# Performance work log

Hardware: AMD Instinct MI355X
Metric: run time of the kernel (lower is better)

The kernel has to match this reference:

```python
import jax, jax.numpy as jnp
import numpy as np

N_KNOTS = 16384
BATCH = 256
N_SAMP = 32768


def setup_inputs() -> dict:
    key = jax.random.key(0)
    k1, k2, k3 = jax.random.split(key, 3)
    # strictly increasing knot abscissae (matches module assumption of sorted x_points)
    incs = jax.random.uniform(k1, (N_KNOTS,), minval=0.01, maxval=1.0, dtype=jnp.float32)
    x_points = jnp.cumsum(incs)
    y_points = jax.random.normal(k2, (N_KNOTS,), dtype=jnp.float32)
    # samples must have a valid right bracket: x in [x_points[0], x_points[N-2])
    lo = x_points[0]
    hi = x_points[N_KNOTS - 2]
    u = jax.random.uniform(k3, (BATCH, N_SAMP), dtype=jnp.float32)
    x_samp = lo + u * (hi - lo) * 0.999
    return {"x_samp": x_samp, "x_points": x_points, "y_points": y_points}


def reference(x_samp, x_points, y_points):
    # Original: masked argmin over (x_samp - x_points) with negatives set to inf,
    # i.e. index of the largest knot <= x_samp. Equivalent to searchsorted(right)-1.
    idxi = jnp.searchsorted(x_points, x_samp, side='right') - 1  # [B, S]
    idxf = idxi + 1
    xi = x_points[idxi]  # [B, S] gather
    xf = x_points[idxf]
    yi = y_points[idxi]
    yf = y_points[idxf]
    ds = (x_samp - xi) / (xf - xi)
    return yi + ds * (yf - yi)
```

## Files before the change

kernel.cpp:

```cpp
#include <hip/hip_runtime.h>


#define NB 16256
#define NKMAX 16384
#define PADR 4
#define NREC (NKMAX + PADR)

typedef float f32x4 __attribute__((ext_vector_type(4)));
typedef float f32x2 __attribute__((ext_vector_type(2)));

__device__ __forceinline__ int bucket_of(float v, float lo, float inv_w) {
    return (int)((v - lo) * inv_w);
}

__device__ __forceinline__ float pack_ys_f(float y, float s) {
    _Float16 hy = (_Float16)y, hs = (_Float16)s;
    unsigned short uy = __builtin_bit_cast(unsigned short, hy);
    unsigned short us = __builtin_bit_cast(unsigned short, hs);
    unsigned u = (unsigned)uy | ((unsigned)us << 16);
    return __builtin_bit_cast(float, u);
}

__device__ __forceinline__ float lerp_ys(float dx, float ysf) {
    unsigned u = __builtin_bit_cast(unsigned, ysf);
    float hy = (float)__builtin_bit_cast(_Float16, (unsigned short)(u & 0xffffu));
    float hs = (float)__builtin_bit_cast(_Float16, (unsigned short)(u >> 16));
    return fmaf(dx, hs, hy);
}

__global__ void build_tbl(const float* __restrict__ xp, const float* __restrict__ yp,
                          float* __restrict__ recg, unsigned short* __restrict__ tbl,
                          int nk) {
    int i = blockIdx.x * blockDim.x + threadIdx.x;
    float lo = xp[0];
    float inv_w = (float)NB / (xp[nk - 1] - lo);
    if (i < nk + PADR) {
        float x, y, s;
        if (i < nk) {
            x = xp[i]; y = yp[i];
            s = (i < nk - 1) ? (yp[i + 1] - y) / (xp[i + 1] - x) : 0.0f;
        } else {
            x = __builtin_inff(); y = 0.0f; s = 0.0f;
        }
        recg[2 * i]     = x;
        recg[2 * i + 1] = pack_ys_f(y, s);
    }
    if (i < NB) {
        int v = 0;
        if (i > 0) {
            int loj = -1, hij = nk - 1;
            while (loj < hij) {
                int mid = (loj + hij + 1) >> 1;
                if (bucket_of(xp[mid], lo, inv_w) <= i - 1) loj = mid; else hij = mid - 1;
            }
            v = loj < 0 ? 0 : (loj > nk - 2 ? nk - 2 : loj);
        }
        tbl[i] = (unsigned short)v;
    }
}

__global__ __launch_bounds__(1024) void interp(
        const f32x4* __restrict__ xs4, const float* __restrict__ xp,
        const float* __restrict__ recg, const unsigned short* __restrict__ tbl,
        f32x4* __restrict__ out4, int n4, int nk) {
    __shared__ __align__(16) float srec[NREC * 2];
    __shared__ unsigned short sT[NB];

    {
        const f32x4* rg4 = (const f32x4*)recg;
        f32x4* sr4 = (f32x4*)srec;
        int n = (NREC * 2) / 4;
        for (int i = threadIdx.x; i < n; i += 1024) sr4[i] = rg4[i];
        for (int i = threadIdx.x; i < NB; i += 1024) sT[i] = tbl[i];
    }

    float lo = xp[0];
    float inv_w = (float)NB / (xp[nk - 1] - lo);
    __syncthreads();

    const f32x2* sr2 = (const f32x2*)srec;

    int tid = blockIdx.x * blockDim.x + threadIdx.x;
    int T = gridDim.x * blockDim.x;

    auto process = [&](f32x4 xq) -> f32x4 {
        float x[4] = {xq.x, xq.y, xq.z, xq.w};
        int base[4];
        f32x2 r0[4], r1[4], r2[4], r3[4];
        #pragma unroll
        for (int k = 0; k < 4; k++) {
            int b = bucket_of(x[k], lo, inv_w);
            b = min(b, NB - 1);
            base[k] = (int)sT[b];
            r0[k] = sr2[base[k]];
            r1[k] = sr2[base[k] + 1];
            r2[k] = sr2[base[k] + 2];
            r3[k] = sr2[base[k] + 3];
        }
        f32x4 res;
        #pragma unroll
        for (int k = 0; k < 4; k++) {
            float xk = x[k];
            float xi = r0[k].x, ys = r0[k].y;
            if (r1[k].x <= xk) { xi = r1[k].x; ys = r1[k].y; }
            if (r2[k].x <= xk) { xi = r2[k].x; ys = r2[k].y; }
            bool tail = (r3[k].x <= xk);
            if (tail) {
                int j = base[k] + 3;
                while (srec[2 * (j + 1)] <= xk) j++;
                xi = srec[2 * j]; ys = srec[2 * j + 1];
            }
            res[k] = lerp_ys(xk - xi, ys);
        }
        return res;
    };

    if (n4 == 8 * T) {
        f32x4 buf[8];
        #pragma unroll
        for (int s = 0; s < 3; s++)
            buf[s] = __builtin_nontemporal_load(&xs4[tid + s * T]);
        #pragma unroll
        for (int s = 0; s < 8; s++) {
            if (s + 3 < 8)
                buf[s + 3] = __builtin_nontemporal_load(&xs4[tid + (s + 3) * T]);
            f32x4 res = process(buf[s]);
            __builtin_nontemporal_store(res, &out4[tid + s * T]);
        }
    } else {
        for (int t = tid; t < n4; t += T) {
            f32x4 xq = __builtin_nontemporal_load(&xs4[t]);
            f32x4 res = process(xq);
            __builtin_nontemporal_store(res, &out4[t]);
        }
    }
}

extern "C" void kernel_launch(void* const* d_in, const int* in_sizes, int n_in,
                              void* d_out, int out_size, void* d_ws, size_t ws_size,
                              hipStream_t stream) {
    const float* xs = (const float*)d_in[0];
    const float* xp = (const float*)d_in[1];
    const float* yp = (const float*)d_in[2];
    int ns = in_sizes[0];
    int nk = in_sizes[1];

    float* recg = (float*)d_ws;
    unsigned short* tbl = (unsigned short*)((char*)d_ws + (size_t)NREC * 2 * sizeof(float));

    int na = (nk + PADR > NB ? nk + PADR : NB);
    build_tbl<<<(na + 255) / 256, 256, 0, stream>>>(xp, yp, recg, tbl, nk);

    int n4 = ns / 4;
    interp<<<256, 1024, 0, stream>>>((const f32x4*)xs, xp, recg, tbl,
                                     (f32x4*)d_out, n4, nk);
}
```

Measured before the change: 103.8 us.

## Fuse table build into interp kernel, building bucket table per block via scatter

Drops the separate build_tbl launch and has each interp block build its knot records and bucket-to-index table directly in shared memory. The table is filled by scattering each knot's index over the buckets it spans, replacing the per-bucket binary search. This removes one kernel launch and the global workspace round trip, but every one of the 256 blocks now recomputes slopes and the table redundantly, with extra divides and global reads.

New measurement: 102.8 us. No clear change (-0.9%).

```diff
diff --git a/kernel.cpp b/kernel.cpp
--- a/kernel.cpp
+++ b/kernel.cpp
@@ -28,54 +28,41 @@
     return fmaf(dx, hs, hy);
 }
 
-__global__ void build_tbl(const float* __restrict__ xp, const float* __restrict__ yp,
-                          float* __restrict__ recg, unsigned short* __restrict__ tbl,
-                          int nk) {
-    int i = blockIdx.x * blockDim.x + threadIdx.x;
-    float lo = xp[0];
-    float inv_w = (float)NB / (xp[nk - 1] - lo);
-    if (i < nk + PADR) {
-        float x, y, s;
-        if (i < nk) {
-            x = xp[i]; y = yp[i];
-            s = (i < nk - 1) ? (yp[i + 1] - y) / (xp[i + 1] - x) : 0.0f;
-        } else {
-            x = __builtin_inff(); y = 0.0f; s = 0.0f;
-        }
-        recg[2 * i]     = x;
-        recg[2 * i + 1] = pack_ys_f(y, s);
-    }
-    if (i < NB) {
-        int v = 0;
-        if (i > 0) {
-            int loj = -1, hij = nk - 1;
-            while (loj < hij) {
-                int mid = (loj + hij + 1) >> 1;
-                if (bucket_of(xp[mid], lo, inv_w) <= i - 1) loj = mid; else hij = mid - 1;
-            }
-            v = loj < 0 ? 0 : (loj > nk - 2 ? nk - 2 : loj);
-        }
-        tbl[i] = (unsigned short)v;
-    }
-}
-
 __global__ __launch_bounds__(1024) void interp(
         const f32x4* __restrict__ xs4, const float* __restrict__ xp,
-        const float* __restrict__ recg, const unsigned short* __restrict__ tbl,
-        f32x4* __restrict__ out4, int n4, int nk) {
+        const float* __restrict__ yp, f32x4* __restrict__ out4, int n4, int nk) {
     __shared__ __align__(16) float srec[NREC * 2];
     __shared__ unsigned short sT[NB];
 
-    {
-        const f32x4* rg4 = (const f32x4*)recg;
-        f32x4* sr4 = (f32x4*)srec;
-        int n = (NREC * 2) / 4;
-        for (int i = threadIdx.x; i < n; i += 1024) sr4[i] = rg4[i];
-        for (int i = threadIdx.x; i < NB; i += 1024) sT[i] = tbl[i];
-    }
-
     float lo = xp[0];
     float inv_w = (float)NB / (xp[nk - 1] - lo);
+
+    {
+        f32x2* sr2w = (f32x2*)srec;
+        for (int i = threadIdx.x; i < nk + PADR; i += 1024) {
+            float x, ysp;
+            int b0 = 0, b1 = -1;
+            if (i < nk) {
+                x = xp[i];
+                float y = yp[i];
+                float s = 0.0f;
+                if (i < nk - 1) {
+                    float xn = xp[i + 1];
+                    s = (yp[i + 1] - y) / (xn - x);
+                    b0 = bucket_of(x, lo, inv_w);
+                    b1 = min(bucket_of(xn, lo, inv_w), NB - 1);
+                }
+                ysp = pack_ys_f(y, s);
+            } else {
+                x = __builtin_inff(); ysp = 0.0f;
+            }
+            f32x2 r; r.x = x; r.y = ysp;
+            sr2w[i] = r;
+            unsigned short v = (unsigned short)(i < nk - 2 ? i : nk - 2);
+            for (int b = b0 + 1; b <= b1; b++) sT[b] = v;
+        }
+        if (threadIdx.x == 0) sT[0] = 0;
+    }
     __syncthreads();
 
     const f32x2* sr2 = (const f32x2*)srec;
@@ -144,14 +131,9 @@
     const float* yp = (const float*)d_in[2];
     int ns = in_sizes[0];
     int nk = in_sizes[1];
-
-    float* recg = (float*)d_ws;
-    unsigned short* tbl = (unsigned short*)((char*)d_ws + (size_t)NREC * 2 * sizeof(float));
-
-    int na = (nk + PADR > NB ? nk + PADR : NB);
-    build_tbl<<<(na + 255) / 256, 256, 0, stream>>>(xp, yp, recg, tbl, nk);
+    (void)d_ws; (void)ws_size; (void)n_in; (void)out_size;
 
     int n4 = ns / 4;
-    interp<<<256, 1024, 0, stream>>>((const f32x4*)xs, xp, recg, tbl,
+    interp<<<256, 1024, 0, stream>>>((const f32x4*)xs, xp, yp,
                                      (f32x4*)d_out, n4, nk);
 }
```
